# Performance work log

Hardware: AMD Instinct MI355X
Metric: run time of the kernel (lower is better)

Reference implementation:

```python
import jax, jax.numpy as jnp
import numpy as np

H = 1024
V = 128000


def setup_inputs() -> dict:
    key = jax.random.key(0)
    ks = jax.random.split(key, 9)
    s = 0.02  # param init scale for numerical sanity
    return {
        "input_ids": jax.random.randint(ks[0], (1,), 0, V),
        "hidden": jax.random.normal(ks[1], (1, 1, H), dtype=jnp.float32),
        "emb": jax.random.normal(ks[2], (V, H), dtype=jnp.float32) * s,
        "W_ih": jax.random.normal(ks[3], (3 * H, H), dtype=jnp.float32) * s,
        "W_hh": jax.random.normal(ks[4], (3 * H, H), dtype=jnp.float32) * s,
        "b_ih": jax.random.normal(ks[5], (3 * H,), dtype=jnp.float32) * s,
        "b_hh": jax.random.normal(ks[6], (3 * H,), dtype=jnp.float32) * s,
        "W_out": jax.random.normal(ks[7], (V, H), dtype=jnp.float32) * s,
        "b_out": jax.random.normal(ks[8], (V,), dtype=jnp.float32) * s,
    }


def reference(input_ids, hidden, emb, W_ih, W_hh, b_ih, b_hh, W_out, b_out):
    # embedding lookup for the single token, then ReLU (matches F.relu on embed)
    x = jax.nn.relu(emb[input_ids[0]])            # (H,)
    h0 = hidden[0, 0]                             # (H,)
    # PyTorch GRU cell: gates ordered [r, z, n]
    gi = W_ih @ x + b_ih                          # (3H,)
    gh = W_hh @ h0 + b_hh                         # (3H,)
    r = jax.nn.sigmoid(gi[:H] + gh[:H])
    z = jax.nn.sigmoid(gi[H:2 * H] + gh[H:2 * H])
    n = jnp.tanh(gi[2 * H:] + r * gh[2 * H:])
    h1 = (1.0 - z) * n + z * h0                   # (H,)
    # output projection + log-softmax over vocab (dim=1 on (1, V))
    logits = W_out @ h1 + b_out                   # (V,)
    logp = jax.nn.log_softmax(logits)[None, :]    # (1, V)
    return logp, h1[None, None, :]                # ((1,V), (1,1,H))
```

## Files before the change

kernel.cpp:

```cpp
#include <hip/hip_runtime.h>
#include <math.h>

#define H 1024
#define V 128000
#define G3H 3072

#define K2_BLOCKS 1024
#define K2_WAVES  (K2_BLOCKS * 4)
#define K2_GROUPS (V / 4)

#define WS_GI   0
#define WS_GH   G3H
#define WS_PART 8192

typedef float f32x4 __attribute__((ext_vector_type(4)));

#define DOT4(w_, x_) fmaf((w_).x,(x_).x, fmaf((w_).y,(x_).y, fmaf((w_).z,(x_).z, (w_).w*(x_).w)))

__global__ __launch_bounds__(256) void gates_matvec(
    const int* __restrict__ ids, const float* __restrict__ hidden,
    const float* __restrict__ emb,
    const float* __restrict__ W_ih, const float* __restrict__ W_hh,
    const float* __restrict__ b_ih, const float* __restrict__ b_hh,
    float* __restrict__ ws) {
  const int tid  = threadIdx.x;
  const int lane = tid & 63;
  const int wid  = blockIdx.x * 4 + (tid >> 6);
  const bool isGi = (wid < 1536);
  const int row0 = (isGi ? wid : wid - 1536) * 2;

  const float* Wm = isGi ? W_ih : W_hh;
  const float* xp = isGi ? (emb + (size_t)ids[0] * H) : hidden;

  f32x4 x0 = ((const f32x4*)xp)[lane];
  f32x4 x1 = ((const f32x4*)xp)[lane + 64];
  f32x4 x2 = ((const f32x4*)xp)[lane + 128];
  f32x4 x3 = ((const f32x4*)xp)[lane + 192];
  if (isGi) {
    x0.x=fmaxf(x0.x,0.f); x0.y=fmaxf(x0.y,0.f); x0.z=fmaxf(x0.z,0.f); x0.w=fmaxf(x0.w,0.f);
    x1.x=fmaxf(x1.x,0.f); x1.y=fmaxf(x1.y,0.f); x1.z=fmaxf(x1.z,0.f); x1.w=fmaxf(x1.w,0.f);
    x2.x=fmaxf(x2.x,0.f); x2.y=fmaxf(x2.y,0.f); x2.z=fmaxf(x2.z,0.f); x2.w=fmaxf(x2.w,0.f);
    x3.x=fmaxf(x3.x,0.f); x3.y=fmaxf(x3.y,0.f); x3.z=fmaxf(x3.z,0.f); x3.w=fmaxf(x3.w,0.f);
  }

  const f32x4* wa = (const f32x4*)(Wm + (size_t)row0 * H);
  const f32x4* wb = (const f32x4*)(Wm + (size_t)(row0 + 1) * H);
  const f32x4 a0 = __builtin_nontemporal_load(wa + lane);
  const f32x4 a1 = __builtin_nontemporal_load(wa + lane + 64);
  const f32x4 a2 = __builtin_nontemporal_load(wa + lane + 128);
  const f32x4 a3 = __builtin_nontemporal_load(wa + lane + 192);
  const f32x4 b0 = __builtin_nontemporal_load(wb + lane);
  const f32x4 b1 = __builtin_nontemporal_load(wb + lane + 64);
  const f32x4 b2 = __builtin_nontemporal_load(wb + lane + 128);
  const f32x4 b3 = __builtin_nontemporal_load(wb + lane + 192);
  float pa = (DOT4(a0,x0) + DOT4(a1,x1)) + (DOT4(a2,x2) + DOT4(a3,x3));
  float pb = (DOT4(b0,x0) + DOT4(b1,x1)) + (DOT4(b2,x2) + DOT4(b3,x3));
#pragma unroll
  for (int off = 1; off < 64; off <<= 1) {
    pa += __shfl_xor(pa, off);
    pb += __shfl_xor(pb, off);
  }
  if (lane < 2) {
    const int row = row0 + lane;
    const float s = (lane == 0) ? pa : pb;
    if (isGi) ws[WS_GI + row] = s + b_ih[row];
    else      ws[WS_GH + row] = s + b_hh[row];
  }
}

__global__ __launch_bounds__(256, 4) void logits_lse(
    const float* __restrict__ hidden, const float* __restrict__ ws_in,
    const float* __restrict__ W_out, const float* __restrict__ b_out,
    float* __restrict__ d_out, float* __restrict__ ws_part) {
  __shared__ __align__(16) float h1s[H];
  const int tid = threadIdx.x;

  for (int i = tid; i < H; i += 256) {
    const float r = 1.f / (1.f + expf(-(ws_in[WS_GI + i]     + ws_in[WS_GH + i])));
    const float z = 1.f / (1.f + expf(-(ws_in[WS_GI + H + i] + ws_in[WS_GH + H + i])));
    const float n = tanhf(ws_in[WS_GI + 2*H + i] + r * ws_in[WS_GH + 2*H + i]);
    h1s[i] = (1.f - z) * n + z * hidden[i];
  }
  __syncthreads();
  if (blockIdx.x == 0) {
    for (int i = tid; i < H; i += 256) d_out[V + i] = h1s[i];
  }

  const int lane = tid & 63;
  const int wid  = blockIdx.x * 4 + (tid >> 6);

  const f32x4 x0 = ((const f32x4*)h1s)[lane];
  const f32x4 x1 = ((const f32x4*)h1s)[lane + 64];
  const f32x4 x2 = ((const f32x4*)h1s)[lane + 128];
  const f32x4 x3 = ((const f32x4*)h1s)[lane + 192];

  float m = -INFINITY, S = 0.f;

#pragma unroll 1
  for (int g = wid; g < K2_GROUPS; g += K2_WAVES) {
    const int row0 = g * 4;
    const f32x4* w = (const f32x4*)(W_out + (size_t)row0 * H);

    const f32x4 a0 = __builtin_nontemporal_load(w + lane);
    const f32x4 a1 = __builtin_nontemporal_load(w + lane + 64);
    const f32x4 a2 = __builtin_nontemporal_load(w + lane + 128);
    const f32x4 a3 = __builtin_nontemporal_load(w + lane + 192);
    const f32x4 b0 = __builtin_nontemporal_load(w + lane + 256);
    const f32x4 b1 = __builtin_nontemporal_load(w + lane + 320);
    const f32x4 b2 = __builtin_nontemporal_load(w + lane + 384);
    const f32x4 b3 = __builtin_nontemporal_load(w + lane + 448);
    const f32x4 c0 = __builtin_nontemporal_load(w + lane + 512);
    const f32x4 c1 = __builtin_nontemporal_load(w + lane + 576);
    const f32x4 c2 = __builtin_nontemporal_load(w + lane + 640);
    const f32x4 c3 = __builtin_nontemporal_load(w + lane + 704);
    const f32x4 d0 = __builtin_nontemporal_load(w + lane + 768);
    const f32x4 d1 = __builtin_nontemporal_load(w + lane + 832);
    const f32x4 d2 = __builtin_nontemporal_load(w + lane + 896);
    const f32x4 d3 = __builtin_nontemporal_load(w + lane + 960);

    float p0 = (DOT4(a0,x0) + DOT4(a1,x1)) + (DOT4(a2,x2) + DOT4(a3,x3));
    float p1 = (DOT4(b0,x0) + DOT4(b1,x1)) + (DOT4(b2,x2) + DOT4(b3,x3));
    float p2 = (DOT4(c0,x0) + DOT4(c1,x1)) + (DOT4(c2,x2) + DOT4(c3,x3));
    float p3 = (DOT4(d0,x0) + DOT4(d1,x1)) + (DOT4(d2,x2) + DOT4(d3,x3));

#pragma unroll
    for (int off = 1; off < 64; off <<= 1) {
      p0 += __shfl_xor(p0, off);
      p1 += __shfl_xor(p1, off);
      p2 += __shfl_xor(p2, off);
      p3 += __shfl_xor(p3, off);
    }

    const float4 bo = *(const float4*)(b_out + row0);
    const float l0 = p0 + bo.x, l1 = p1 + bo.y, l2 = p2 + bo.z, l3 = p3 + bo.w;

    const float sel = (lane == 0) ? l0 : (lane == 1) ? l1 : (lane == 2) ? l2 : l3;
    if (lane < 4) d_out[row0 + lane] = sel;

    const float m4 = fmaxf(fmaxf(l0, l1), fmaxf(l2, l3));
    const float mn = fmaxf(m, m4);
    S = S * expf(m - mn)
      + expf(l0 - mn) + expf(l1 - mn) + expf(l2 - mn) + expf(l3 - mn);
    m = mn;
  }

  if (lane == 0) {
    ws_part[2*wid]     = m;
    ws_part[2*wid + 1] = S;
  }
}

__global__ __launch_bounds__(256) void lse_norm(
    float* __restrict__ d_out, const float* __restrict__ ws_part) {
  __shared__ float redm[256], reds[256];
  const int tid = threadIdx.x;

  float m = -INFINITY, S = 0.f;
  for (int b = tid; b < K2_WAVES; b += 256) {
    const float mb = ws_part[2*b], sb = ws_part[2*b+1];
    const float mn = fmaxf(m, mb);
    S = S * expf(m - mn) + sb * expf(mb - mn);
    m = mn;
  }
  redm[tid] = m; reds[tid] = S;
  __syncthreads();
  for (int s = 128; s > 0; s >>= 1) {
    if (tid < s) {
      const float m2 = redm[tid + s], s2 = reds[tid + s];
      const float mn = fmaxf(redm[tid], m2);
      reds[tid] = reds[tid] * expf(redm[tid] - mn) + s2 * expf(m2 - mn);
      redm[tid] = mn;
    }
    __syncthreads();
  }
  const float lse = redm[0] + logf(reds[0]);

  const int i = blockIdx.x * 256 + tid;
  d_out[i] -= lse;
}

extern "C" void kernel_launch(void* const* d_in, const int* in_sizes, int n_in,
                              void* d_out, int out_size, void* d_ws, size_t ws_size,
                              hipStream_t stream) {
  const int*   ids    = (const int*)d_in[0];
  const float* hidden = (const float*)d_in[1];
  const float* emb    = (const float*)d_in[2];
  const float* W_ih   = (const float*)d_in[3];
  const float* W_hh   = (const float*)d_in[4];
  const float* b_ih   = (const float*)d_in[5];
  const float* b_hh   = (const float*)d_in[6];
  const float* W_out  = (const float*)d_in[7];
  const float* b_out  = (const float*)d_in[8];
  float* out = (float*)d_out;
  float* ws  = (float*)d_ws;

  gates_matvec<<<768, 256, 0, stream>>>(ids, hidden, emb, W_ih, W_hh, b_ih, b_hh, ws);
  logits_lse<<<K2_BLOCKS, 256, 0, stream>>>(hidden, ws, W_out, b_out, out, ws + WS_PART);
  lse_norm<<<500, 256, 0, stream>>>(out, ws + WS_PART);
}
```

Before: 102.7 us.

## Use contiguous row ranges per wave, block-level LSE partials, fast exp intrinsics

```diff
diff --git a/kernel.cpp b/kernel.cpp
--- a/kernel.cpp
+++ b/kernel.cpp
@@ -8,6 +8,7 @@
 #define K2_BLOCKS 1024
 #define K2_WAVES  (K2_BLOCKS * 4)
 #define K2_GROUPS (V / 4)
+#define NPART     K2_BLOCKS
 
 #define WS_GI   0
 #define WS_GH   G3H
@@ -16,6 +17,13 @@
 typedef float f32x4 __attribute__((ext_vector_type(4)));
 
 #define DOT4(w_, x_) fmaf((w_).x,(x_).x, fmaf((w_).y,(x_).y, fmaf((w_).z,(x_).z, (w_).w*(x_).w)))
+
+__device__ __forceinline__ float sigmoid_fast(float x) {
+  return 1.f / (1.f + __expf(-x));
+}
+__device__ __forceinline__ float tanh_fast(float x) {
+  return 1.f - 2.f / (__expf(2.f * x) + 1.f);
+}
 
 __global__ __launch_bounds__(256) void gates_matvec(
     const int* __restrict__ ids, const float* __restrict__ hidden,
@@ -72,32 +80,48 @@
     const float* __restrict__ hidden, const float* __restrict__ ws_in,
     const float* __restrict__ W_out, const float* __restrict__ b_out,
     float* __restrict__ d_out, float* __restrict__ ws_part) {
-  __shared__ __align__(16) float h1s[H];
+  __shared__ __align__(16) f32x4 h1s4[256];
+  __shared__ float wpm[4], wps[4];
   const int tid = threadIdx.x;
 
-  for (int i = tid; i < H; i += 256) {
-    const float r = 1.f / (1.f + expf(-(ws_in[WS_GI + i]     + ws_in[WS_GH + i])));
-    const float z = 1.f / (1.f + expf(-(ws_in[WS_GI + H + i] + ws_in[WS_GH + H + i])));
-    const float n = tanhf(ws_in[WS_GI + 2*H + i] + r * ws_in[WS_GH + 2*H + i]);
-    h1s[i] = (1.f - z) * n + z * hidden[i];
+  {
+    const f32x4* ws4 = (const f32x4*)ws_in;
+    const f32x4 gi0 = ws4[tid];
+    const f32x4 gi1 = ws4[tid + 256];
+    const f32x4 gi2 = ws4[tid + 512];
+    const f32x4 gh0 = ws4[tid + 768];
+    const f32x4 gh1 = ws4[tid + 1024];
+    const f32x4 gh2 = ws4[tid + 1280];
+    const f32x4 h0v = ((const f32x4*)hidden)[tid];
+    f32x4 h1;
+#pragma unroll
+    for (int j = 0; j < 4; ++j) {
+      const float r = sigmoid_fast(gi0[j] + gh0[j]);
+      const float z = sigmoid_fast(gi1[j] + gh1[j]);
+      const float n = tanh_fast(gi2[j] + r * gh2[j]);
+      h1[j] = (1.f - z) * n + z * h0v[j];
+    }
+    h1s4[tid] = h1;
   }
   __syncthreads();
   if (blockIdx.x == 0) {
-    for (int i = tid; i < H; i += 256) d_out[V + i] = h1s[i];
+    ((f32x4*)(d_out + V))[tid] = h1s4[tid];
   }
 
   const int lane = tid & 63;
   const int wid  = blockIdx.x * 4 + (tid >> 6);
-
-  const f32x4 x0 = ((const f32x4*)h1s)[lane];
-  const f32x4 x1 = ((const f32x4*)h1s)[lane + 64];
-  const f32x4 x2 = ((const f32x4*)h1s)[lane + 128];
-  const f32x4 x3 = ((const f32x4*)h1s)[lane + 192];
+  const int gbeg = (wid * K2_GROUPS) >> 12;
+  const int gend = ((wid + 1) * K2_GROUPS) >> 12;
+
+  const f32x4 x0 = h1s4[lane];
+  const f32x4 x1 = h1s4[lane + 64];
+  const f32x4 x2 = h1s4[lane + 128];
+  const f32x4 x3 = h1s4[lane + 192];
 
   float m = -INFINITY, S = 0.f;
 
 #pragma unroll 1
-  for (int g = wid; g < K2_GROUPS; g += K2_WAVES) {
+  for (int g = gbeg; g < gend; ++g) {
     const int row0 = g * 4;
     const f32x4* w = (const f32x4*)(W_out + (size_t)row0 * H);
 
@@ -139,14 +163,24 @@
 
     const float m4 = fmaxf(fmaxf(l0, l1), fmaxf(l2, l3));
     const float mn = fmaxf(m, m4);
-    S = S * expf(m - mn)
-      + expf(l0 - mn) + expf(l1 - mn) + expf(l2 - mn) + expf(l3 - mn);
+    S = S * __expf(m - mn)
+      + __expf(l0 - mn) + __expf(l1 - mn) + __expf(l2 - mn) + __expf(l3 - mn);
     m = mn;
   }
 
-  if (lane == 0) {
-    ws_part[2*wid]     = m;
-    ws_part[2*wid + 1] = S;
+  if (lane == 0) { wpm[tid >> 6] = m; wps[tid >> 6] = S; }
+  __syncthreads();
+  if (tid == 0) {
+    float bm = wpm[0], bS = wps[0];
+#pragma unroll
+    for (int k = 1; k < 4; ++k) {
+      const float mk = wpm[k], sk = wps[k];
+      const float mn = fmaxf(bm, mk);
+      bS = bS * __expf(bm - mn) + sk * __expf(mk - mn);
+      bm = mn;
+    }
+    ws_part[2 * blockIdx.x]     = bm;
+    ws_part[2 * blockIdx.x + 1] = bS;
   }
 }
 
@@ -156,10 +190,10 @@
   const int tid = threadIdx.x;
 
   float m = -INFINITY, S = 0.f;
-  for (int b = tid; b < K2_WAVES; b += 256) {
+  for (int b = tid; b < NPART; b += 256) {
     const float mb = ws_part[2*b], sb = ws_part[2*b+1];
     const float mn = fmaxf(m, mb);
-    S = S * expf(m - mn) + sb * expf(mb - mn);
+    S = S * __expf(m - mn) + sb * __expf(mb - mn);
     m = mn;
   }
   redm[tid] = m; reds[tid] = S;
@@ -168,7 +202,7 @@
     if (tid < s) {
       const float m2 = redm[tid + s], s2 = reds[tid + s];
       const float mn = fmaxf(redm[tid], m2);
-      reds[tid] = reds[tid] * expf(redm[tid] - mn) + s2 * expf(m2 - mn);
+      reds[tid] = reds[tid] * __expf(redm[tid] - mn) + s2 * __expf(m2 - mn);
       redm[tid] = mn;
     }
     __syncthreads();
```

Result: faster. 97.09 us (median of 2 runs) (-5.5%).
